# Optimization experiments

Measured on AMD Instinct MI355X. Metric: run time of the kernel, lower is better.

The kernel has to match this reference:

```python
import jax, jax.numpy as jnp
import numpy as np

EMBED_DIM = 1024
HEAD_SIZE = 128
B, S = 8, 2048

def setup_inputs() -> dict:
    rng = jax.random.key(0)
    k1, k2, k3, k4, k5, k6 = jax.random.split(rng, 6)
    std = 1.0 / EMBED_DIM  # nn.initializers.normal(stddev=1/embed_dim)
    return {
        "key": jax.random.normal(k1, (B, S, EMBED_DIM), dtype=jnp.float32),
        "query": jax.random.normal(k2, (B, S, EMBED_DIM), dtype=jnp.float32),
        "value": jax.random.normal(k3, (B, S, EMBED_DIM), dtype=jnp.float32),
        "W_Q": jax.random.normal(k4, (EMBED_DIM, HEAD_SIZE), dtype=jnp.float32) * std,
        "W_K": jax.random.normal(k5, (EMBED_DIM, HEAD_SIZE), dtype=jnp.float32) * std,
        "W_V": jax.random.normal(k6, (EMBED_DIM, HEAD_SIZE), dtype=jnp.float32) * std,
    }

def reference(key, query, value, W_Q, W_K, W_V):
    # Parallel retention: (Q K^T * causal_mask) V
    q_proj = query @ W_Q        # (B, S, H)
    k_proj = key @ W_K          # (B, S, H)
    v_proj = value @ W_V        # (B, S, H)
    ret = jnp.einsum("bsh,bth->bst", q_proj, k_proj)  # (B, S, S)
    # full_self_retention=False -> lower-triangular (causal) mask
    decay_matrix = jnp.tril(jnp.ones((S, S), dtype=ret.dtype))
    ret = ret * decay_matrix
    return ret @ v_proj          # (B, S, H)
```

## Files before the change

kernel.cpp:

```cpp
#include <hip/hip_runtime.h>
#include <cstdint>

#define B_  8
#define S_  2048
#define E_  1024
#define H_  128
#define NC_ 16

typedef __attribute__((ext_vector_type(8))) short bf16x8;
typedef __attribute__((ext_vector_type(4))) float f32x4;

__device__ __forceinline__ short f2bf(float f){
  uint32_t u = __builtin_bit_cast(uint32_t, f);
  u = (u + 0x7fffu + ((u >> 16) & 1u)) >> 16;
  return (short)u;
}
__device__ __forceinline__ float bf2f(short s){
  uint32_t u = ((uint32_t)(uint16_t)s) << 16;
  return __builtin_bit_cast(float, u);
}
__device__ __forceinline__ void load_lds16(const void* g, void* l){
  __builtin_amdgcn_global_load_lds(
    (const __attribute__((address_space(1))) void*)g,
    (__attribute__((address_space(3))) void*)l, 16, 0, 0);
}

__global__ __launch_bounds__(256) void wt_kernel(
    const float* __restrict__ WQ, const float* __restrict__ WK,
    const float* __restrict__ WV,
    short* __restrict__ WtQ, short* __restrict__ WtK, short* __restrict__ WtV)
{
  int which = blockIdx.z;
  const float* W = which == 0 ? WQ : which == 1 ? WK : WV;
  short* Wt      = which == 0 ? WtQ : which == 1 ? WtK : WtV;
  int k0 = blockIdx.x * 32, n0 = blockIdx.y * 32;
  __shared__ float t[32][33];
  int tx = threadIdx.x & 31, ty = threadIdx.x >> 5;
  #pragma unroll
  for (int i = 0; i < 4; i++)
    t[ty + i * 8][tx] = W[(size_t)(k0 + ty + i * 8) * H_ + n0 + tx];
  __syncthreads();
  #pragma unroll
  for (int i = 0; i < 4; i++)
    Wt[(size_t)(n0 + ty + i * 8) * E_ + k0 + tx] = f2bf(t[tx][ty + i * 8]);
}

__global__ __launch_bounds__(256) void proj_kernel(
    const float* __restrict__ Xq, const float* __restrict__ Xk,
    const float* __restrict__ Xv,
    const short* __restrict__ Wtq, const short* __restrict__ Wtk,
    const short* __restrict__ Wtv,
    short* __restrict__ q, short* __restrict__ k,
    short* __restrict__ kT, short* __restrict__ vT)
{
  int which = blockIdx.y;
  const float* X  = which == 0 ? Xq  : which == 1 ? Xk  : Xv;
  const short* Wt = which == 0 ? Wtq : which == 1 ? Wtk : Wtv;

  int tid = threadIdx.x, lane = tid & 63, wave = tid >> 6;
  int lr = lane & 15, lq = lane >> 4;
  int rowbase = blockIdx.x * 64 + wave * 16;

  __shared__ short Bs[2][128 * 40];

  const float* xr = X + (size_t)(rowbase + lr) * E_ + lq * 8;
  int bn = tid >> 1, bc = (tid & 1) * 16;
  const short* wsrc = Wt + (size_t)bn * E_ + bc;

  f32x4 acc[8];
  #pragma unroll
  for (int tn = 0; tn < 8; tn++) acc[tn] = (f32x4){0.f, 0.f, 0.f, 0.f};

  f32x4 alo = *(const f32x4*)xr;
  f32x4 ahi = *(const f32x4*)(xr + 4);
  *(bf16x8*)(&Bs[0][bn * 40 + bc])     = *(const bf16x8*)wsrc;
  *(bf16x8*)(&Bs[0][bn * 40 + bc + 8]) = *(const bf16x8*)(wsrc + 8);
  __syncthreads();

  int p = 0;
  for (int k0 = 0; k0 < E_; k0 += 32){
    bool more = (k0 + 32) < E_;
    f32x4 nlo, nhi; bf16x8 nb0, nb1;
    if (more){
      nlo = *(const f32x4*)(xr + k0 + 32);
      nhi = *(const f32x4*)(xr + k0 + 36);
      nb0 = *(const bf16x8*)(wsrc + k0 + 32);
      nb1 = *(const bf16x8*)(wsrc + k0 + 40);
    }
    bf16x8 a;
    #pragma unroll
    for (int j = 0; j < 4; j++){ a[j] = f2bf(alo[j]); a[4 + j] = f2bf(ahi[j]); }
    #pragma unroll
    for (int tn = 0; tn < 8; tn++){
      bf16x8 bfr = *(const bf16x8*)(&Bs[p][(tn * 16 + lr) * 40 + lq * 8]);
      acc[tn] = __builtin_amdgcn_mfma_f32_16x16x32_bf16(a, bfr, acc[tn], 0, 0, 0);
    }
    if (more){
      *(bf16x8*)(&Bs[p ^ 1][bn * 40 + bc])     = nb0;
      *(bf16x8*)(&Bs[p ^ 1][bn * 40 + bc + 8]) = nb1;
      __syncthreads();
      alo = nlo; ahi = nhi; p ^= 1;
    }
  }

  if (which <= 1){
    short* P = which == 0 ? q : k;
    #pragma unroll
    for (int tn = 0; tn < 8; tn++)
      #pragma unroll
      for (int r4 = 0; r4 < 4; r4++)
        P[(size_t)(rowbase + lq * 4 + r4) * H_ + tn * 16 + lr] = f2bf(acc[tn][r4]);
  }
  if (which >= 1){
    short* T = which == 1 ? kT : vT;
    int b = rowbase >> 11, s = rowbase & 2047;
    #pragma unroll
    for (int tn = 0; tn < 8; tn++){
      union { short sh[4]; uint2 u; } pk;
      #pragma unroll
      for (int r4 = 0; r4 < 4; r4++) pk.sh[r4] = f2bf(acc[tn][r4]);
      *(uint2*)(T + ((size_t)b * H_ + tn * 16 + lr) * S_ + s + lq * 4) = pk.u;
    }
  }
}

__global__ __launch_bounds__(256) void chunk_state(
    const short* __restrict__ vT, const short* __restrict__ kT,
    float* __restrict__ M)
{
  int j = blockIdx.x, half = blockIdx.y, b = blockIdx.z;
  int tid = threadIdx.x, lane = tid & 63, wave = tid >> 6;
  int wrow = wave * 32;
  int lr = lane & 15, lq = lane >> 4;

  __shared__ short As[128 * 32];
  __shared__ short Bs[64 * 32];

  const short* vtb = vT + (size_t)b * H_ * S_ + j * 128;
  const short* ktb = kT + (size_t)b * H_ * S_ + (size_t)half * 64 * S_ + j * 128;

  f32x4 acc[2][4];
  #pragma unroll
  for (int a = 0; a < 2; a++)
    #pragma unroll
    for (int c = 0; c < 4; c++) acc[a][c] = (f32x4){0.f, 0.f, 0.f, 0.f};

  for (int t0 = 0; t0 < 128; t0 += 32){
    __syncthreads();
    #pragma unroll
    for (int i = 0; i < 2; i++){
      int r = wave * 32 + i * 16 + (lane >> 2);
      int c = (lane & 3) * 8;
      load_lds16(vtb + (size_t)r * S_ + t0 + c,
                 (void*)(As + (wave * 32 + i * 16) * 32));
    }
    {
      int r = wave * 16 + (lane >> 2);
      int c = (lane & 3) * 8;
      load_lds16(ktb + (size_t)r * S_ + t0 + c,
                 (void*)(Bs + (wave * 16) * 32));
    }
    __syncthreads();
    bf16x8 af[2], bf[4];
    #pragma unroll
    for (int tm = 0; tm < 2; tm++)
      af[tm] = *(const bf16x8*)(As + (wrow + tm * 16 + lr) * 32 + lq * 8);
    #pragma unroll
    for (int tn = 0; tn < 4; tn++)
      bf[tn] = *(const bf16x8*)(Bs + (tn * 16 + lr) * 32 + lq * 8);
    #pragma unroll
    for (int tm = 0; tm < 2; tm++)
      #pragma unroll
      for (int tn = 0; tn < 4; tn++)
        acc[tm][tn] = __builtin_amdgcn_mfma_f32_16x16x32_bf16(
            af[tm], bf[tn], acc[tm][tn], 0, 0, 0);
  }

  float* mb = M + (size_t)(b * NC_ + j) * 16384;
  #pragma unroll
  for (int tm = 0; tm < 2; tm++)
    #pragma unroll
    for (int tn = 0; tn < 4; tn++)
      #pragma unroll
      for (int r4 = 0; r4 < 4; r4++){
        int row = wrow + tm * 16 + lq * 4 + r4;
        int col = half * 64 + tn * 16 + lr;
        mb[row * 128 + col] = acc[tm][tn][r4];
      }
}

__global__ __launch_bounds__(256) void prefix_state(
    const float* __restrict__ M, short* __restrict__ Shi, short* __restrict__ Slo)
{
  int b = blockIdx.y;
  int idx = (blockIdx.x * 256 + threadIdx.x) * 4;
  float4 mv[NC_];
  #pragma unroll
  for (int j = 0; j < NC_; j++)
    mv[j] = *(const float4*)(M + (size_t)(b * NC_ + j) * 16384 + idx);

  float r0 = 0.f, r1 = 0.f, r2 = 0.f, r3 = 0.f;
  #pragma unroll
  for (int j = 0; j < NC_; j++){
    size_t o = (size_t)(b * NC_ + j) * 16384 + idx;
    short h0 = f2bf(r0), h1 = f2bf(r1), h2 = f2bf(r2), h3 = f2bf(r3);
    short l0 = f2bf(r0 - bf2f(h0)), l1 = f2bf(r1 - bf2f(h1));
    short l2 = f2bf(r2 - bf2f(h2)), l3 = f2bf(r3 - bf2f(h3));
    union { short s[4]; uint2 u; } ph, pl;
    ph.s[0] = h0; ph.s[1] = h1; ph.s[2] = h2; ph.s[3] = h3;
    pl.s[0] = l0; pl.s[1] = l1; pl.s[2] = l2; pl.s[3] = l3;
    *(uint2*)(Shi + o) = ph.u;
    *(uint2*)(Slo + o) = pl.u;
    r0 += mv[j].x; r1 += mv[j].y; r2 += mv[j].z; r3 += mv[j].w;
  }
}

__global__ __launch_bounds__(256) void passC(
    const short* __restrict__ qb, const short* __restrict__ kb,
    const short* __restrict__ vT, const short* __restrict__ Shi,
    const short* __restrict__ Slo, float* __restrict__ out)
{
  int i = blockIdx.x, half = blockIdx.y, b = blockIdx.z;
  int roff = half * 64;
  int tid = threadIdx.x, lane = tid & 63, wave = tid >> 6;
  int wrow = (wave >> 1) * 32, wcol = (wave & 1) * 64;
  int lr = lane & 15, lq = lane >> 4;

  __shared__ short Qs[64 * 136];
  __shared__ short Ss[64 * 136];
  __shared__ short Bsh[128 * 32];

  const short* qbase = qb + ((size_t)b * S_ + i * 128 + roff) * H_;
  const short* kbase = kb + ((size_t)b * S_ + i * 128) * H_;
  const short* vtb   = vT + (size_t)b * H_ * S_ + i * 128;
  const short* shib  = Shi + (size_t)(b * NC_ + i) * 16384;
  const short* slob  = Slo + (size_t)(b * NC_ + i) * 16384;

  #pragma unroll
  for (int t = 0; t < 4; t++){
    int chunk = t * 256 + tid;
    int s = chunk >> 4, c16 = chunk & 15;
    *(uint4*)(Qs + s * 136 + c16 * 8) =
        *(const uint4*)(qbase + s * H_ + c16 * 8);
  }

  f32x4 acc[2][4];
  #pragma unroll
  for (int a = 0; a < 2; a++)
    #pragma unroll
    for (int c = 0; c < 4; c++) acc[a][c] = (f32x4){0.f, 0.f, 0.f, 0.f};

  for (int h0 = 0; h0 < H_; h0 += 32){
    __syncthreads();
    #pragma unroll
    for (int t = 0; t < 2; t++){
      int r = wave * 32 + t * 16 + (lane >> 2);
      int c = (lane & 3) * 8;
      load_lds16(kbase + (size_t)r * H_ + h0 + c,
                 (void*)(Bsh + (wave * 32 + t * 16) * 32));
    }
    __syncthreads();
    bf16x8 af[2], bf[4];
    #pragma unroll
    for (int tm = 0; tm < 2; tm++)
      af[tm] = *(const bf16x8*)(Qs + (wrow + tm * 16 + lr) * 136 + h0 + lq * 8);
    #pragma unroll
    for (int tn = 0; tn < 4; tn++)
      bf[tn] = *(const bf16x8*)(Bsh + (wcol + tn * 16 + lr) * 32 + lq * 8);
    #pragma unroll
    for (int tm = 0; tm < 2; tm++)
      #pragma unroll
      for (int tn = 0; tn < 4; tn++)
        acc[tm][tn] = __builtin_amdgcn_mfma_f32_16x16x32_bf16(
            af[tm], bf[tn], acc[tm][tn], 0, 0, 0);
  }
  __syncthreads();

  #pragma unroll
  for (int tm = 0; tm < 2; tm++)
    #pragma unroll
    for (int tn = 0; tn < 4; tn++)
      #pragma unroll
      for (int r4 = 0; r4 < 4; r4++){
        int row = wrow + tm * 16 + lq * 4 + r4;
        int col = wcol + tn * 16 + lr;
        float vv = (col <= roff + row) ? acc[tm][tn][r4] : 0.f;
        Ss[row * 136 + col] = f2bf(vv);
      }
  #pragma unroll
  for (int a = 0; a < 2; a++)
    #pragma unroll
    for (int c = 0; c < 4; c++) acc[a][c] = (f32x4){0.f, 0.f, 0.f, 0.f};
  __syncthreads();

  for (int t0 = 0; t0 < 128; t0 += 32){
    __syncthreads();
    #pragma unroll
    for (int t = 0; t < 2; t++){
      int r = wave * 32 + t * 16 + (lane >> 2);
      int c = (lane & 3) * 8;
      load_lds16(vtb + (size_t)r * S_ + t0 + c,
                 (void*)(Bsh + (wave * 32 + t * 16) * 32));
    }
    __syncthreads();
    bf16x8 af[2], bf[4];
    #pragma unroll
    for (int tm = 0; tm < 2; tm++)
      af[tm] = *(const bf16x8*)(Ss + (wrow + tm * 16 + lr) * 136 + t0 + lq * 8);
    #pragma unroll
    for (int tn = 0; tn < 4; tn++)
      bf[tn] = *(const bf16x8*)(Bsh + (wcol + tn * 16 + lr) * 32 + lq * 8);
    #pragma unroll
    for (int tm = 0; tm < 2; tm++)
      #pragma unroll
      for (int tn = 0; tn < 4; tn++)
        acc[tm][tn] = __builtin_amdgcn_mfma_f32_16x16x32_bf16(
            af[tm], bf[tn], acc[tm][tn], 0, 0, 0);
  }

  #pragma unroll
  for (int part = 0; part < 2; part++){
    const short* sb = part == 0 ? shib : slob;
    for (int h0 = 0; h0 < H_; h0 += 32){
      __syncthreads();
      #pragma unroll
      for (int t = 0; t < 2; t++){
        int r = wave * 32 + t * 16 + (lane >> 2);
        int c = (lane & 3) * 8;
        load_lds16(sb + (size_t)r * 128 + h0 + c,
                   (void*)(Bsh + (wave * 32 + t * 16) * 32));
      }
      __syncthreads();
      bf16x8 af[2], bf[4];
      #pragma unroll
      for (int tm = 0; tm < 2; tm++)
        af[tm] = *(const bf16x8*)(Qs + (wrow + tm * 16 + lr) * 136 + h0 + lq * 8);
      #pragma unroll
      for (int tn = 0; tn < 4; tn++)
        bf[tn] = *(const bf16x8*)(Bsh + (wcol + tn * 16 + lr) * 32 + lq * 8);
      #pragma unroll
      for (int tm = 0; tm < 2; tm++)
        #pragma unroll
        for (int tn = 0; tn < 4; tn++)
          acc[tm][tn] = __builtin_amdgcn_mfma_f32_16x16x32_bf16(
              af[tm], bf[tn], acc[tm][tn], 0, 0, 0);
    }
  }

  float* ob = out + ((size_t)b * S_ + i * 128 + roff) * H_;
  #pragma unroll
  for (int tm = 0; tm < 2; tm++)
    #pragma unroll
    for (int tn = 0; tn < 4; tn++)
      #pragma unroll
      for (int r4 = 0; r4 < 4; r4++){
        int row = wrow + tm * 16 + lq * 4 + r4;
        int col = wcol + tn * 16 + lr;
        ob[(size_t)row * H_ + col] = acc[tm][tn][r4];
      }
}

extern "C" void kernel_launch(void* const* d_in, const int* in_sizes, int n_in,
                              void* d_out, int out_size, void* d_ws, size_t ws_size,
                              hipStream_t stream) {
  const float* key   = (const float*)d_in[0];
  const float* query = (const float*)d_in[1];
  const float* value = (const float*)d_in[2];
  const float* WQ    = (const float*)d_in[3];
  const float* WK    = (const float*)d_in[4];
  const float* WV    = (const float*)d_in[5];
  float* out = (float*)d_out;

  char* w = (char*)d_ws;
  short* WtQ = (short*)(w + 0);
  short* WtK = (short*)(w + 262144);
  short* WtV = (short*)(w + 524288);
  size_t o = 786432;
  short* q  = (short*)(w + o); o += 4194304;
  short* k  = (short*)(w + o); o += 4194304;
  short* kT = (short*)(w + o); o += 4194304;
  short* vT = (short*)(w + o); o += 4194304;
  float* M  = (float*)(w + o); o += 8388608;
  short* Shi= (short*)(w + o); o += 4194304;
  short* Slo= (short*)(w + o); o += 4194304;

  wt_kernel   <<<dim3(32, 4, 3),       256, 0, stream>>>(WQ, WK, WV, WtQ, WtK, WtV);
  proj_kernel <<<dim3(256, 3),         256, 0, stream>>>(query, key, value,
                                                         WtQ, WtK, WtV, q, k, kT, vT);
  chunk_state <<<dim3(NC_, 2, B_),     256, 0, stream>>>(vT, kT, M);
  prefix_state<<<dim3(16, B_),         256, 0, stream>>>(M, Shi, Slo);
  passC       <<<dim3(NC_, 2, B_),     256, 0, stream>>>(q, k, vT, Shi, Slo, out);
}
```

Before: 248.8 us.

## Stage full 128-wide tiles in padded LDS instead of 32-wide k-steps

Replaces the 32-wide K-step loops that used direct global-to-LDS loads with one bulk vectorized load of a full 128-column tile into padded (136-stride) LDS. This is done in the projection, chunk-state and passC kernels, cutting the number of barriers and load rounds. In passC, Q fragments are now held in registers for both the intra-chunk and state matmuls, so the Qs LDS buffer is dropped. The cost is more LDS per block, which may reduce occupancy, and the projection kernel loses its register double-buffering, so global-load latency is less hidden.

```diff
diff --git a/kernel.cpp b/kernel.cpp
--- a/kernel.cpp
+++ b/kernel.cpp
@@ -18,11 +18,6 @@
 __device__ __forceinline__ float bf2f(short s){
   uint32_t u = ((uint32_t)(uint16_t)s) << 16;
   return __builtin_bit_cast(float, u);
-}
-__device__ __forceinline__ void load_lds16(const void* g, void* l){
-  __builtin_amdgcn_global_load_lds(
-    (const __attribute__((address_space(1))) void*)g,
-    (__attribute__((address_space(3))) void*)l, 16, 0, 0);
 }
 
 __global__ __launch_bounds__(256) void wt_kernel(
@@ -61,45 +56,42 @@
   int lr = lane & 15, lq = lane >> 4;
   int rowbase = blockIdx.x * 64 + wave * 16;
 
-  __shared__ short Bs[2][128 * 40];
+  __shared__ short Bs[128 * 136];
 
   const float* xr = X + (size_t)(rowbase + lr) * E_ + lq * 8;
-  int bn = tid >> 1, bc = (tid & 1) * 16;
-  const short* wsrc = Wt + (size_t)bn * E_ + bc;
 
   f32x4 acc[8];
   #pragma unroll
   for (int tn = 0; tn < 8; tn++) acc[tn] = (f32x4){0.f, 0.f, 0.f, 0.f};
 
-  f32x4 alo = *(const f32x4*)xr;
-  f32x4 ahi = *(const f32x4*)(xr + 4);
-  *(bf16x8*)(&Bs[0][bn * 40 + bc])     = *(const bf16x8*)wsrc;
-  *(bf16x8*)(&Bs[0][bn * 40 + bc + 8]) = *(const bf16x8*)(wsrc + 8);
-  __syncthreads();
-
-  int p = 0;
-  for (int k0 = 0; k0 < E_; k0 += 32){
-    bool more = (k0 + 32) < E_;
-    f32x4 nlo, nhi; bf16x8 nb0, nb1;
-    if (more){
-      nlo = *(const f32x4*)(xr + k0 + 32);
-      nhi = *(const f32x4*)(xr + k0 + 36);
-      nb0 = *(const bf16x8*)(wsrc + k0 + 32);
-      nb1 = *(const bf16x8*)(wsrc + k0 + 40);
-    }
-    bf16x8 a;
-    #pragma unroll
-    for (int j = 0; j < 4; j++){ a[j] = f2bf(alo[j]); a[4 + j] = f2bf(ahi[j]); }
-    #pragma unroll
-    for (int tn = 0; tn < 8; tn++){
-      bf16x8 bfr = *(const bf16x8*)(&Bs[p][(tn * 16 + lr) * 40 + lq * 8]);
-      acc[tn] = __builtin_amdgcn_mfma_f32_16x16x32_bf16(a, bfr, acc[tn], 0, 0, 0);
-    }
-    if (more){
-      *(bf16x8*)(&Bs[p ^ 1][bn * 40 + bc])     = nb0;
-      *(bf16x8*)(&Bs[p ^ 1][bn * 40 + bc + 8]) = nb1;
-      __syncthreads();
-      alo = nlo; ahi = nhi; p ^= 1;
+  for (int kc = 0; kc < 8; kc++){
+    if (kc) __syncthreads();
+    #pragma unroll
+    for (int v = 0; v < 8; v++){
+      int c = v * 256 + tid;
+      int n = c >> 4, off = (c & 15) * 8;
+      *(bf16x8*)(&Bs[n * 136 + off]) =
+          *(const bf16x8*)(Wt + (size_t)n * E_ + kc * 128 + off);
+    }
+    f32x4 ar[8];
+    #pragma unroll
+    for (int s = 0; s < 4; s++){
+      ar[2 * s]     = *(const f32x4*)(xr + kc * 128 + s * 32);
+      ar[2 * s + 1] = *(const f32x4*)(xr + kc * 128 + s * 32 + 4);
+    }
+    __syncthreads();
+    #pragma unroll
+    for (int s = 0; s < 4; s++){
+      bf16x8 a;
+      #pragma unroll
+      for (int j = 0; j < 4; j++){
+        a[j] = f2bf(ar[2 * s][j]); a[4 + j] = f2bf(ar[2 * s + 1][j]);
+      }
+      #pragma unroll
+      for (int tn = 0; tn < 8; tn++){
+        bf16x8 bfr = *(const bf16x8*)(&Bs[(tn * 16 + lr) * 136 + s * 32 + lq * 8]);
+        acc[tn] = __builtin_amdgcn_mfma_f32_16x16x32_bf16(a, bfr, acc[tn], 0, 0, 0);
+      }
     }
   }
 
@@ -133,41 +125,42 @@
   int wrow = wave * 32;
   int lr = lane & 15, lq = lane >> 4;
 
-  __shared__ short As[128 * 32];
-  __shared__ short Bs[64 * 32];
+  __shared__ short As[128 * 136];
+  __shared__ short Bs[64 * 136];
 
   const short* vtb = vT + (size_t)b * H_ * S_ + j * 128;
   const short* ktb = kT + (size_t)b * H_ * S_ + (size_t)half * 64 * S_ + j * 128;
 
+  #pragma unroll
+  for (int v = 0; v < 8; v++){
+    int c = v * 256 + tid;
+    int r = c >> 4, off = (c & 15) * 8;
+    *(bf16x8*)(&As[r * 136 + off]) = *(const bf16x8*)(vtb + (size_t)r * S_ + off);
+  }
+  #pragma unroll
+  for (int v = 0; v < 4; v++){
+    int c = v * 256 + tid;
+    int r = c >> 4, off = (c & 15) * 8;
+    *(bf16x8*)(&Bs[r * 136 + off]) = *(const bf16x8*)(ktb + (size_t)r * S_ + off);
+  }
+  __syncthreads();
+
   f32x4 acc[2][4];
   #pragma unroll
   for (int a = 0; a < 2; a++)
     #pragma unroll
     for (int c = 0; c < 4; c++) acc[a][c] = (f32x4){0.f, 0.f, 0.f, 0.f};
 
-  for (int t0 = 0; t0 < 128; t0 += 32){
-    __syncthreads();
-    #pragma unroll
-    for (int i = 0; i < 2; i++){
-      int r = wave * 32 + i * 16 + (lane >> 2);
-      int c = (lane & 3) * 8;
-      load_lds16(vtb + (size_t)r * S_ + t0 + c,
-                 (void*)(As + (wave * 32 + i * 16) * 32));
-    }
-    {
-      int r = wave * 16 + (lane >> 2);
-      int c = (lane & 3) * 8;
-      load_lds16(ktb + (size_t)r * S_ + t0 + c,
-                 (void*)(Bs + (wave * 16) * 32));
-    }
-    __syncthreads();
+  #pragma unroll
+  for (int s = 0; s < 4; s++){
+    int t0 = s * 32;
     bf16x8 af[2], bf[4];
     #pragma unroll
     for (int tm = 0; tm < 2; tm++)
-      af[tm] = *(const bf16x8*)(As + (wrow + tm * 16 + lr) * 32 + lq * 8);
-    #pragma unroll
-    for (int tn = 0; tn < 4; tn++)
-      bf[tn] = *(const bf16x8*)(Bs + (tn * 16 + lr) * 32 + lq * 8);
+      af[tm] = *(const bf16x8*)(&As[(wrow + tm * 16 + lr) * 136 + t0 + lq * 8]);
+    #pragma unroll
+    for (int tn = 0; tn < 4; tn++)
+      bf[tn] = *(const bf16x8*)(&Bs[(tn * 16 + lr) * 136 + t0 + lq * 8]);
     #pragma unroll
     for (int tm = 0; tm < 2; tm++)
       #pragma unroll
@@ -226,9 +219,8 @@
   int wrow = (wave >> 1) * 32, wcol = (wave & 1) * 64;
   int lr = lane & 15, lq = lane >> 4;
 
-  __shared__ short Qs[64 * 136];
   __shared__ short Ss[64 * 136];
-  __shared__ short Bsh[128 * 32];
+  __shared__ short Bt[128 * 136];
 
   const short* qbase = qb + ((size_t)b * S_ + i * 128 + roff) * H_;
   const short* kbase = kb + ((size_t)b * S_ + i * 128) * H_;
@@ -236,13 +228,21 @@
   const short* shib  = Shi + (size_t)(b * NC_ + i) * 16384;
   const short* slob  = Slo + (size_t)(b * NC_ + i) * 16384;
 
-  #pragma unroll
-  for (int t = 0; t < 4; t++){
-    int chunk = t * 256 + tid;
-    int s = chunk >> 4, c16 = chunk & 15;
-    *(uint4*)(Qs + s * 136 + c16 * 8) =
-        *(const uint4*)(qbase + s * H_ + c16 * 8);
-  }
+  bf16x8 aq[2][4];
+  #pragma unroll
+  for (int tm = 0; tm < 2; tm++)
+    #pragma unroll
+    for (int hs = 0; hs < 4; hs++)
+      aq[tm][hs] = *(const bf16x8*)(
+          qbase + (size_t)(wrow + tm * 16 + lr) * H_ + hs * 32 + lq * 8);
+
+  #pragma unroll
+  for (int v = 0; v < 8; v++){
+    int c = v * 256 + tid;
+    int r = c >> 4, off = (c & 15) * 8;
+    *(bf16x8*)(&Bt[r * 136 + off]) = *(const bf16x8*)(kbase + (size_t)r * H_ + off);
+  }
+  __syncthreads();
 
   f32x4 acc[2][4];
   #pragma unroll
@@ -250,29 +250,18 @@
     #pragma unroll
     for (int c = 0; c < 4; c++) acc[a][c] = (f32x4){0.f, 0.f, 0.f, 0.f};
 
-  for (int h0 = 0; h0 < H_; h0 += 32){
-    __syncthreads();
-    #pragma unroll
-    for (int t = 0; t < 2; t++){
-      int r = wave * 32 + t * 16 + (lane >> 2);
-      int c = (lane & 3) * 8;
-      load_lds16(kbase + (size_t)r * H_ + h0 + c,
-                 (void*)(Bsh + (wave * 32 + t * 16) * 32));
-    }
-    __syncthreads();
-    bf16x8 af[2], bf[4];
-    #pragma unroll
-    for (int tm = 0; tm < 2; tm++)
-      af[tm] = *(const bf16x8*)(Qs + (wrow + tm * 16 + lr) * 136 + h0 + lq * 8);
-    #pragma unroll
-    for (int tn = 0; tn < 4; tn++)
-      bf[tn] = *(const bf16x8*)(Bsh + (wcol + tn * 16 + lr) * 32 + lq * 8);
+  #pragma unroll
+  for (int hs = 0; hs < 4; hs++){
+    bf16x8 bf[4];
+    #pragma unroll
+    for (int tn = 0; tn < 4; tn++)
+      bf[tn] = *(const bf16x8*)(&Bt[(wcol + tn * 16 + lr) * 136 + hs * 32 + lq * 8]);
     #pragma unroll
     for (int tm = 0; tm < 2; tm++)
       #pragma unroll
       for (int tn = 0; tn < 4; tn++)
         acc[tm][tn] = __builtin_amdgcn_mfma_f32_16x16x32_bf16(
-            af[tm], bf[tn], acc[tm][tn], 0, 0, 0);
+            aq[tm][hs], bf[tn], acc[tm][tn], 0, 0, 0);
   }
   __syncthreads();
 
@@ -288,28 +277,27 @@
         Ss[row * 136 + col] = f2bf(vv);
       }
   #pragma unroll
+  for (int v = 0; v < 8; v++){
+    int c = v * 256 + tid;
+    int r = c >> 4, off = (c & 15) * 8;
+    *(bf16x8*)(&Bt[r * 136 + off]) = *(const bf16x8*)(vtb + (size_t)r * S_ + off);
+  }
+  #pragma unroll
   for (int a = 0; a < 2; a++)
     #pragma unroll
     for (int c = 0; c < 4; c++) acc[a][c] = (f32x4){0.f, 0.f, 0.f, 0.f};
   __syncthreads();
 
-  for (int t0 = 0; t0 < 128; t0 += 32){
-    __syncthreads();
-    #pragma unroll
-    for (int t = 0; t < 2; t++){
-      int r = wave * 32 + t * 16 + (lane >> 2);
-      int c = (lane & 3) * 8;
-      load_lds16(vtb + (size_t)r * S_ + t0 + c,
-                 (void*)(Bsh + (wave * 32 + t * 16) * 32));
-    }
-    __syncthreads();
+  #pragma unroll
+  for (int s = 0; s < 4; s++){
+    int t0 = s * 32;
     bf16x8 af[2], bf[4];
     #pragma unroll
     for (int tm = 0; tm < 2; tm++)
-      af[tm] = *(const bf16x8*)(Ss + (wrow + tm * 16 + lr) * 136 + t0 + lq * 8);
-    #pragma unroll
-    for (int tn = 0; tn < 4; tn++)
-      bf[tn] = *(const bf16x8*)(Bsh + (wcol + tn * 16 + lr) * 32 + lq * 8);
+      af[tm] = *(const bf16x8*)(&Ss[(wrow + tm * 16 + lr) * 136 + t0 + lq * 8]);
+    #pragma unroll
+    for (int tn = 0; tn < 4; tn++)
+      bf[tn] = *(const bf16x8*)(&Bt[(wcol + tn * 16 + lr) * 136 + t0 + lq * 8]);
     #pragma unroll
     for (int tm = 0; tm < 2; tm++)
       #pragma unroll
@@ -317,34 +305,32 @@
         acc[tm][tn] = __builtin_amdgcn_mfma_f32_16x16x32_bf16(
             af[tm], bf[tn], acc[tm][tn], 0, 0, 0);
   }
+  __syncthreads();
 
   #pragma unroll
   for (int part = 0; part < 2; part++){
     const short* sb = part == 0 ? shib : slob;
-    for (int h0 = 0; h0 < H_; h0 += 32){
-      __syncthreads();
-      #pragma unroll
-      for (int t = 0; t < 2; t++){
-        int r = wave * 32 + t * 16 + (lane >> 2);
-        int c = (lane & 3) * 8;
-        load_lds16(sb + (size_t)r * 128 + h0 + c,
-                   (void*)(Bsh + (wave * 32 + t * 16) * 32));
-      }
-      __syncthreads();
-      bf16x8 af[2], bf[4];
-      #pragma unroll
-      for (int tm = 0; tm < 2; tm++)
-        af[tm] = *(const bf16x8*)(Qs + (wrow + tm * 16 + lr) * 136 + h0 + lq * 8);
+    #pragma unroll
+    for (int v = 0; v < 8; v++){
+      int c = v * 256 + tid;
+      int r = c >> 4, off = (c & 15) * 8;
+      *(bf16x8*)(&Bt[r * 136 + off]) = *(const bf16x8*)(sb + (size_t)r * 128 + off);
+    }
+    __syncthreads();
+    #pragma unroll
+    for (int hs = 0; hs < 4; hs++){
+      bf16x8 bf[4];
       #pragma unroll
       for (int tn = 0; tn < 4; tn++)
-        bf[tn] = *(const bf16x8*)(Bsh + (wcol + tn * 16 + lr) * 32 + lq * 8);
+        bf[tn] = *(const bf16x8*)(&Bt[(wcol + tn * 16 + lr) * 136 + hs * 32 + lq * 8]);
       #pragma unroll
       for (int tm = 0; tm < 2; tm++)
         #pragma unroll
         for (int tn = 0; tn < 4; tn++)
           acc[tm][tn] = __builtin_amdgcn_mfma_f32_16x16x32_bf16(
-              af[tm], bf[tn], acc[tm][tn], 0, 0, 0);
-    }
+              aq[tm][hs], bf[tn], acc[tm][tn], 0, 0, 0);
+    }
+    if (part == 0) __syncthreads();
   }
 
   float* ob = out + ((size_t)b * S_ + i * 128 + roff) * H_;
```

Result: faster. 228.6 us (-8.1%).
